# Kernel tuning notes

Measured on AMD Instinct MI355X. Metric: run time of the kernel, lower is better.

The kernel has to match this reference:

```python
import jax, jax.numpy as jnp
import numpy as np
import math

D = 64; H = 4; HD = 16; NL = 2; K = 3; FUT = 12; HID = 128
B = 8192; N = 16; L = 4; F = 7

def _linear(x, w, b):
    return x @ w.T + b

def _ln(x, g, b):
    m = x.mean(-1, keepdims=True)
    v = ((x - m) ** 2).mean(-1, keepdims=True)
    return (x - m) / jnp.sqrt(v + 1e-5) * g + b

def _mha(q, kv, in_w, in_b, out_w, out_b):
    # torch nn.MultiheadAttention: packed in_proj [Wq;Wk;Wv], averaged attn weights
    wq, wk, wv = in_w[:D], in_w[D:2*D], in_w[2*D:]
    bq, bk, bv = in_b[:D], in_b[D:2*D], in_b[2*D:]
    Bq, Lq, _ = q.shape; Lk = kv.shape[1]
    Q = (_linear(q, wq, bq)).reshape(Bq, Lq, H, HD)
    Kh = (_linear(kv, wk, bk)).reshape(Bq, Lk, H, HD)
    V = (_linear(kv, wv, bv)).reshape(Bq, Lk, H, HD)
    s = jnp.einsum('bqhd,bkhd->bhqk', Q, Kh) / math.sqrt(HD)
    a = jax.nn.softmax(s, axis=-1)
    o = jnp.einsum('bhqk,bkhd->bqhd', a, V).reshape(Bq, Lq, D)
    return _linear(o, out_w, out_b), a.mean(axis=1)

def _encode(tok, pe, embed_w, embed_b, layers):
    aiw, aib, aow, aob, f1w, f1b, f2w, f2b, l1g, l1b, l2g, l2b = layers
    x = _linear(tok, embed_w, embed_b) + pe[:, :tok.shape[1], :]
    for i in range(NL):
        a, _ = _mha(x, x, aiw[i], aib[i], aow[i], aob[i])
        x = _ln(x + a, l1g[i], l1b[i])
        f = _linear(jax.nn.relu(_linear(x, f1w[i], f1b[i])), f2w[i], f2b[i])
        x = _ln(x + f, l2g[i], l2b[i])
    return x[:, -1, :]

def _make_pe():
    pe = np.zeros((100, D), dtype=np.float32)
    pos = np.arange(100, dtype=np.float32)[:, None]
    div = np.exp(np.arange(0, D, 2, dtype=np.float32) * (-math.log(10000.0) / D))
    pe[:, 0::2] = np.sin(pos * div)
    pe[:, 1::2] = np.cos(pos * div)
    return jnp.asarray(pe[None])

def setup_inputs() -> dict:
    key = jax.random.key(0)
    ks = iter(jax.random.split(key, 40))
    p = lambda shape: jax.random.normal(next(ks), shape, dtype=jnp.float32) * 0.05
    inp = {
        'x': jax.random.normal(next(ks), (B, L, F), dtype=jnp.float32),
        'neighbors': jax.random.normal(next(ks), (B, N, L, F), dtype=jnp.float32),
        'pe': _make_pe(),
        'embed_w': p((D, F)), 'embed_b': p((D,)),
        'attn_in_w': p((NL, 3*D, D)), 'attn_in_b': p((NL, 3*D)),
        'attn_out_w': p((NL, D, D)), 'attn_out_b': p((NL, D)),
        'ff1_w': p((NL, 256, D)), 'ff1_b': p((NL, 256)),
        'ff2_w': p((NL, D, 256)), 'ff2_b': p((NL, D)),
        'ln1_g': jnp.ones((NL, D)), 'ln1_b': jnp.zeros((NL, D)),
        'ln2_g': jnp.ones((NL, D)), 'ln2_b': jnp.zeros((NL, D)),
        'soc_in_w': p((3*D, D)), 'soc_in_b': p((3*D,)),
        'soc_out_w': p((D, D)), 'soc_out_b': p((D,)),
        'goal1_w': p((64, HID)), 'goal1_b': p((64,)),
        'goal2_w': p((K*2, 64)), 'goal2_b': p((K*2,)),
        'traj1_w': p((128, HID + 2)), 'traj1_b': p((128,)),
        'traj2_w': p((FUT*2, 128)), 'traj2_b': p((FUT*2,)),
        'prob_w': p((K, HID)), 'prob_b': p((K,)),
    }
    return inp

def reference(x, neighbors, pe, embed_w, embed_b, attn_in_w, attn_in_b, attn_out_w, attn_out_b,
              ff1_w, ff1_b, ff2_w, ff2_b, ln1_g, ln1_b, ln2_g, ln2_b,
              soc_in_w, soc_in_b, soc_out_w, soc_out_b,
              goal1_w, goal1_b, goal2_w, goal2_b, traj1_w, traj1_b, traj2_w, traj2_b,
              prob_w, prob_b):
    b, n, l, f = neighbors.shape
    layers = (attn_in_w, attn_in_b, attn_out_w, attn_out_b, ff1_w, ff1_b, ff2_w, ff2_b,
              ln1_g, ln1_b, ln2_g, ln2_b)
    h = _encode(x, pe, embed_w, embed_b, layers)                       # (B, D) target last-token
    nh = _encode(neighbors.reshape(b*n, l, f), pe, embed_w, embed_b, layers).reshape(b, n, D)
    soc, attn_w = _mha(h[:, None, :], nh, soc_in_w, soc_in_b, soc_out_w, soc_out_b)
    h_final = jnp.concatenate([h, soc[:, 0, :]], axis=-1)              # (B, 128)
    goals = _linear(jax.nn.relu(_linear(h_final, goal1_w, goal1_b)), goal2_w, goal2_b).reshape(b, K, 2)
    cond = jnp.concatenate([jnp.broadcast_to(h_final[:, None, :], (b, K, HID)), goals], axis=-1)
    traj = _linear(jax.nn.relu(_linear(cond, traj1_w, traj1_b)), traj2_w, traj2_b).reshape(b, K, FUT, 2)
    probs = jax.nn.softmax(_linear(h_final, prob_w, prob_b), axis=-1)
    return traj, goals, probs, attn_w
```

## Files before the change

### kernel.cpp

```cpp
#include <hip/hip_runtime.h>

typedef __attribute__((ext_vector_type(8))) short short8;
typedef __attribute__((ext_vector_type(4))) float f32x4;

#define B_EGO 8192
#define NSEQ  139264

#define WS_CONST 0
#define WS_SIN   2432
#define WS_SOUT  14720
#define WS_G1    18816
#define WS_G2    27008
#define WS_T1    27392
#define WS_T1T   43776
#define WS_T2    44032
#define WS_PROB  47104
#define WS_H     47488
#define WS_NH    571776
#define PACK_F   8960384
#define PACK_HL  49152
#define PACK_PER_LAYER 98304

#define OUT_TRAJ  0
#define OUT_GOALS (B_EGO*72)
#define OUT_PROBS (OUT_GOALS + B_EGO*6)
#define OUT_ATTN  (OUT_PROBS + B_EGO*3)

#define MFMA(a,b,c) __builtin_amdgcn_mfma_f32_16x16x32_bf16(a,b,c,0,0,0)

__device__ __forceinline__ float dot4(float4 a, float4 b) {
  return a.x*b.x + a.y*b.y + a.z*b.z + a.w*b.w;
}
__device__ __forceinline__ unsigned short f2bf(float f) {
  unsigned int u = __float_as_uint(f);
  return (unsigned short)((u + 0x7FFFu + ((u >> 16) & 1u)) >> 16);
}
__device__ __forceinline__ float bfval(unsigned short h) {
  return __uint_as_float(((unsigned int)h) << 16);
}
__device__ __forceinline__ void pksplit(float a, float b,
                                        unsigned int& hi, unsigned int& lo) {
  unsigned int ua = __float_as_uint(a), ub = __float_as_uint(b);
  hi = (ua >> 16) | (ub & 0xFFFF0000u);
  float ra = a - __uint_as_float(ua & 0xFFFF0000u);
  float rb = b - __uint_as_float(ub & 0xFFFF0000u);
  unsigned short al = f2bf(ra), bl = f2bf(rb);
  lo = (unsigned int)al | ((unsigned int)bl << 16);
}
__device__ __forceinline__ short8 mkfrag(unsigned int a, unsigned int b,
                                         unsigned int c, unsigned int d) {
  union { short8 s; unsigned int w[4]; } u;
  u.w[0] = a; u.w[1] = b; u.w[2] = c; u.w[3] = d;
  return u.s;
}

__global__ void prep_consts(
    const float* __restrict__ embed_w, const float* __restrict__ embed_b,
    const float* __restrict__ pe,
    const float* __restrict__ attn_in_b, const float* __restrict__ attn_out_b,
    const float* __restrict__ ff1_b, const float* __restrict__ ff2_b,
    const float* __restrict__ ln1_g, const float* __restrict__ ln1_b,
    const float* __restrict__ ln2_g, const float* __restrict__ ln2_b,
    float* __restrict__ wsF)
{
  int idx = blockIdx.x * 256 + threadIdx.x;
  if (idx >= 2432) return;
  float v;
  if (idx < 448)      { int f = idx >> 6, c = idx & 63; v = embed_w[c*7 + f]; }
  else if (idx < 512) { v = embed_b[idx - 448]; }
  else if (idx < 768) { v = pe[idx - 512]; }
  else {
    int i = idx - 768, l = i / 832, j = i - l*832;
    if      (j < 192) v = attn_in_b [l*192 + j];
    else if (j < 256) v = attn_out_b[l*64  + j - 192];
    else if (j < 512) v = ff1_b     [l*256 + j - 256];
    else if (j < 576) v = ff2_b     [l*64  + j - 512];
    else if (j < 640) v = ln1_g     [l*64  + j - 576];
    else if (j < 704) v = ln1_b     [l*64  + j - 640];
    else if (j < 768) v = ln2_g     [l*64  + j - 704];
    else              v = ln2_b     [l*64  + j - 768];
  }
  wsF[idx] = v;
}

__global__ void prep_social(
    const float* __restrict__ soc_in_w, const float* __restrict__ soc_out_w,
    const float* __restrict__ goal1_w,  const float* __restrict__ goal2_w,
    const float* __restrict__ traj1_w,  const float* __restrict__ traj2_w,
    const float* __restrict__ prob_w,   float* __restrict__ wsF)
{
  int idx = blockIdx.x * 256 + threadIdx.x;
  if (idx >= 45056) return;
  float v; int t, i;
  if (idx < 12288) { t = idx; i = t & 3; t >>= 2; int o = t % 192, dc = t / 192;
    v = soc_in_w[o*64 + dc*4 + i]; }
  else if (idx < 16384) { t = idx - 12288; i = t & 3; t >>= 2; int o = t & 63, dc = t >> 6;
    v = soc_out_w[o*64 + dc*4 + i]; }
  else if (idx < 24576) { t = idx - 16384; i = t & 3; t >>= 2; int o = t & 63, dc = t >> 6;
    v = goal1_w[o*128 + dc*4 + i]; }
  else if (idx < 24960) { t = idx - 24576; i = t & 3; t >>= 2; int o = t % 6, dc = t / 6;
    v = goal2_w[o*64 + dc*4 + i]; }
  else if (idx < 41344) { t = idx - 24960; i = t & 3; t >>= 2; int o = t & 127, dc = t >> 7;
    v = traj1_w[o*130 + dc*4 + i]; }
  else if (idx < 41600) { t = idx - 41344; int o = t >> 1, j = t & 1;
    v = traj1_w[o*130 + 128 + j]; }
  else if (idx < 44672) { t = idx - 41600; i = t & 3; t >>= 2; int o = t % 24, dc = t / 24;
    v = traj2_w[o*128 + dc*4 + i]; }
  else { t = idx - 44672; i = t & 3; t >>= 2; int o = t % 3, dc = t / 3;
    v = prob_w[o*128 + dc*4 + i]; }
  wsF[WS_SIN + idx] = v;
}

__global__ void prep_mfma(
    const float* __restrict__ attn_in_w, const float* __restrict__ attn_out_w,
    const float* __restrict__ ff1_w,     const float* __restrict__ ff2_w,
    float* __restrict__ wsF)
{
  int idx = blockIdx.x * 256 + threadIdx.x;
  unsigned short* pw = (unsigned short*)(wsF + PACK_F);
  int l = idx / PACK_HL, r = idx - l*PACK_HL;
  int e = r & 7, lane = (r >> 3) & 63;
  int g = lane >> 4, l15 = lane & 15;
  float v;
  if (r < 12288) {
    int which = r >> 12;
    int ks = (r >> 9) & 1, t = (r >> 10) & 3;
    int c = (e & 3)*16 + ks*8 + 4*(e >> 2) + g;
    v = attn_in_w[l*12288 + (which*64 + t*16 + l15)*64 + c];
  } else if (r < 16384) {
    int r2 = r - 12288; int ks = (r2 >> 9) & 1, t = r2 >> 10;
    int c = ks*32 + g*4 + (e & 3) + 16*(e >> 2);
    v = attn_out_w[l*4096 + (t*16 + l15)*64 + c];
  } else if (r < 32768) {
    int r2 = r - 16384; int ks = (r2 >> 9) & 1, mt = r2 >> 10;
    int c = (e & 3)*16 + ks*8 + 4*(e >> 2) + g;
    v = ff1_w[l*16384 + (mt*16 + l15)*64 + c];
  } else {
    int r2 = r - 32768; int ks = (r2 >> 9) & 7, t = r2 >> 12;
    int c = ks*32 + g*4 + (e & 3) + 16*(e >> 2);
    v = ff2_w[l*16384 + (t*16 + l15)*256 + c];
  }
  unsigned short hw = f2bf(v);
  unsigned short lw = f2bf(v - bfval(hw));
  pw[l*PACK_PER_LAYER + r]           = hw;
  pw[l*PACK_PER_LAYER + PACK_HL + r] = lw;
}

__device__ __forceinline__ void lnorm(f32x4 xr[4], const float* cls,
                                      int gof, int bof, int l15) {
  float mean[4], rs[4];
  #pragma unroll
  for (int reg = 0; reg < 4; ++reg) {
    float s1 = xr[0][reg] + xr[1][reg] + xr[2][reg] + xr[3][reg];
    float s2 = xr[0][reg]*xr[0][reg] + xr[1][reg]*xr[1][reg]
             + xr[2][reg]*xr[2][reg] + xr[3][reg]*xr[3][reg];
    #pragma unroll
    for (int off = 1; off < 16; off <<= 1) {
      s1 += __shfl_xor(s1, off);
      s2 += __shfl_xor(s2, off);
    }
    float m = s1 * 0.015625f;
    float v = fmaxf(s2 * 0.015625f - m*m, 0.f);
    mean[reg] = m; rs[reg] = rsqrtf(v + 1e-5f);
  }
  #pragma unroll
  for (int t = 0; t < 4; ++t) {
    float gg = cls[gof + t*16 + l15], bb = cls[bof + t*16 + l15];
    #pragma unroll
    for (int reg = 0; reg < 4; ++reg)
      xr[t][reg] = (xr[t][reg] - mean[reg]) * rs[reg] * gg + bb;
  }
}

__device__ __forceinline__ void writeX(char* xbh, char* xbl,
                                       const f32x4 xr[4], int g, int l15) {
  #pragma unroll
  for (int reg = 0; reg < 4; ++reg) {
    int r = g*4 + reg;
    uint2 vh, vl;
    pksplit(xr[0][reg], xr[1][reg], vh.x, vl.x);
    pksplit(xr[2][reg], xr[3][reg], vh.y, vl.y);
    int off = (r*128 + l15*8) ^ ((r & 7) << 4);
    *(uint2*)(xbh + off) = vh;
    *(uint2*)(xbl + off) = vl;
  }
}

__device__ __forceinline__ void readX(const char* xbh, const char* xbl,
                                      short8 xah[2], short8 xal[2],
                                      int g, int l15) {
  #pragma unroll
  for (int ks = 0; ks < 2; ++ks) {
    int o1 = (l15*128 + ks*64 + g*8)      ^ ((l15 & 7) << 4);
    int o2 = (l15*128 + ks*64 + g*8 + 32) ^ ((l15 & 7) << 4);
    union { short8 s; uint2 d[2]; } uh, ul;
    uh.d[0] = *(const uint2*)(xbh + o1); uh.d[1] = *(const uint2*)(xbh + o2);
    ul.d[0] = *(const uint2*)(xbl + o1); ul.d[1] = *(const uint2*)(xbl + o2);
    xah[ks] = uh.s; xal[ks] = ul.s;
  }
}

__device__ __forceinline__ void splitA(const f32x4 a, const f32x4 b,
                                       short8& fh, short8& fl) {
  unsigned int w0, w1, w2, w3, z0, z1, z2, z3;
  pksplit(a[0], a[1], w0, z0);
  pksplit(a[2], a[3], w1, z1);
  pksplit(b[0], b[1], w2, z2);
  pksplit(b[2], b[3], w3, z3);
  fh = mkfrag(w0, w1, w2, w3);
  fl = mkfrag(z0, z1, z2, z3);
}

__global__ __launch_bounds__(256) void encode_kernel(
    const float* __restrict__ xin, const float* __restrict__ nbr,
    const float* __restrict__ wsF, float* __restrict__ hout)
{
  __shared__ __align__(16) float cls[2432];
  __shared__ float tok_ls[4][112];
  __shared__ __align__(16) unsigned short xs[4][2048];

  const int tid = threadIdx.x;
  const int w = tid >> 6, lane = tid & 63;
  const int g = lane >> 4, l15 = lane & 15;
  const f32x4 zero = {0.f, 0.f, 0.f, 0.f};

  for (int i = tid; i < 2432; i += 256) cls[i] = wsF[i];

  const int seq0w = blockIdx.x * 16 + w * 4;
  {
    const float* tokp = (blockIdx.x < 512) ? (xin + seq0w*28)
                                           : (nbr + (seq0w - B_EGO)*28);
    tok_ls[w][lane] = tokp[lane];
    if (lane < 48) tok_ls[w][64 + lane] = tokp[64 + lane];
  }
  __syncthreads();

  char* xbh = (char*)(xs[w]);
  char* xbl = xbh + 2048;
  const unsigned short* pw = (const unsigned short*)(wsF + PACK_F);

  f32x4 xr[4];
  {
    float tk[4][7];
    #pragma unroll
    for (int reg = 0; reg < 4; ++reg)
      #pragma unroll
      for (int f = 0; f < 7; ++f)
        tk[reg][f] = tok_ls[w][g*28 + reg*7 + f];
    #pragma unroll
    for (int t = 0; t < 4; ++t) {
      const int c = t*16 + l15;
      float we[7];
      #pragma unroll
      for (int f = 0; f < 7; ++f) we[f] = cls[f*64 + c];
      const float ebv = cls[448 + c];
      #pragma unroll
      for (int reg = 0; reg < 4; ++reg) {
        float acc = ebv + cls[512 + reg*64 + c];
        #pragma unroll
        for (int f = 0; f < 7; ++f) acc = fmaf(tk[reg][f], we[f], acc);
        xr[t][reg] = acc;
      }
    }
  }
  writeX(xbh, xbl, xr, g, l15);

  #pragma unroll 1
  for (int ly = 0; ly < 2; ++ly) {
    const unsigned short* PLh = pw + ly*PACK_PER_LAYER;
    const unsigned short* PLl = PLh + PACK_HL;
    const int lb = 768 + ly*832;
    short8 xah[2], xal[2];
    readX(xbh, xbl, xah, xal, g, l15);

    f32x4 q4[4], k4[4], v4[4];
    #pragma unroll
    for (int t = 0; t < 4; ++t) {
      q4[t] = zero; k4[t] = zero; v4[t] = zero;
      #pragma unroll
      for (int ks = 0; ks < 2; ++ks) {
        const int wo = ((t*2+ks)*64 + lane)*8;
        short8 aqh = *(const short8*)(PLh + wo);
        short8 aql = *(const short8*)(PLl + wo);
        short8 akh = *(const short8*)(PLh + 4096 + wo);
        short8 akl = *(const short8*)(PLl + 4096 + wo);
        short8 bvh = *(const short8*)(PLh + 8192 + wo);
        short8 bvl = *(const short8*)(PLl + 8192 + wo);
        q4[t] = MFMA(aql, xah[ks], MFMA(aqh, xal[ks], MFMA(aqh, xah[ks], q4[t])));
        k4[t] = MFMA(akl, xah[ks], MFMA(akh, xal[ks], MFMA(akh, xah[ks], k4[t])));
        v4[t] = MFMA(xal[ks], bvh, MFMA(xah[ks], bvl, MFMA(xah[ks], bvh, v4[t])));
      }
      f32x4 bq = *(const f32x4*)(&cls[lb +      t*16 + g*4]);
      f32x4 bk = *(const f32x4*)(&cls[lb + 64 + t*16 + g*4]);
      q4[t] += bq; k4[t] += bk;
      float bvv = cls[lb + 128 + t*16 + l15];
      #pragma unroll
      for (int j = 0; j < 4; ++j) v4[t][j] += bvv;
    }

    f32x4 oacc[4];
    const float vmask = (g == (l15 >> 2)) ? 1.f : 0.f;
    #pragma unroll
    for (int h = 0; h < 4; ++h) {
      short8 aKh, aKl, bQh, bQl;
      splitA(k4[h], zero, aKh, aKl);
      splitA(q4[h], zero, bQh, bQl);
      f32x4 sa = MFMA(aKl, bQh, MFMA(aKh, bQl, MFMA(aKh, bQh, zero)));
      float s0 = sa[0]*0.25f, s1 = sa[1]*0.25f, s2 = sa[2]*0.25f, s3 = sa[3]*0.25f;
      float mx = fmaxf(fmaxf(s0, s1), fmaxf(s2, s3));
      float e0 = __expf(s0-mx), e1 = __expf(s1-mx), e2 = __expf(s2-mx), e3 = __expf(s3-mx);
      float inv = vmask / (e0 + e1 + e2 + e3);
      f32x4 pv = {e0*inv, e1*inv, e2*inv, e3*inv};
      short8 aVh, aVl, bPh, bPl;
      splitA(v4[h], zero, aVh, aVl);
      splitA(pv,    zero, bPh, bPl);
      oacc[h] = MFMA(aVl, bPh, MFMA(aVh, bPl, MFMA(aVh, bPh, zero)));
    }

    short8 aOh[2], aOl[2];
    #pragma unroll
    for (int ks = 0; ks < 2; ++ks)
      splitA(oacc[2*ks], oacc[2*ks+1], aOh[ks], aOl[ks]);
    #pragma unroll
    for (int t = 0; t < 4; ++t) {
      f32x4 fa = zero;
      #pragma unroll
      for (int ks = 0; ks < 2; ++ks) {
        const int wo = 12288 + ((t*2+ks)*64 + lane)*8;
        short8 bOh = *(const short8*)(PLh + wo);
        short8 bOl = *(const short8*)(PLl + wo);
        fa = MFMA(aOl[ks], bOh, MFMA(aOh[ks], bOl, MFMA(aOh[ks], bOh, fa)));
      }
      float bo = cls[lb + 192 + t*16 + l15];
      #pragma unroll
      for (int j = 0; j < 4; ++j) xr[t][j] += fa[j] + bo;
    }
    lnorm(xr, cls, lb + 576, lb + 640, l15);

    writeX(xbh, xbl, xr, g, l15);
    readX(xbh, xbl, xah, xal, g, l15);

    f32x4 h16[16];
    #pragma unroll
    for (int mt = 0; mt < 16; ++mt) {
      h16[mt] = zero;
      #pragma unroll
      for (int ks = 0; ks < 2; ++ks) {
        const int wo = 16384 + ((mt*2+ks)*64 + lane)*8;
        short8 a1h = *(const short8*)(PLh + wo);
        short8 a1l = *(const short8*)(PLl + wo);
        h16[mt] = MFMA(a1l, xah[ks], MFMA(a1h, xal[ks], MFMA(a1h, xah[ks], h16[mt])));
      }
      f32x4 b1 = *(const f32x4*)(&cls[lb + 256 + mt*16 + g*4]);
      #pragma unroll
      for (int j = 0; j < 4; ++j) h16[mt][j] = fmaxf(h16[mt][j] + b1[j], 0.f);
    }

    f32x4 f2[4] = {zero, zero, zero, zero};
    #pragma unroll
    for (int ks = 0; ks < 8; ++ks) {
      short8 aHh, aHl;
      splitA(h16[2*ks], h16[2*ks+1], aHh, aHl);
      #pragma unroll
      for (int t = 0; t < 4; ++t) {
        const int wo = 32768 + ((t*8+ks)*64 + lane)*8;
        short8 b2h = *(const short8*)(PLh + wo);
        short8 b2l = *(const short8*)(PLl + wo);
        f2[t] = MFMA(aHl, b2h, MFMA(aHh, b2l, MFMA(aHh, b2h, f2[t])));
      }
    }
    #pragma unroll
    for (int t = 0; t < 4; ++t) {
      float b2v = cls[lb + 512 + t*16 + l15];
      #pragma unroll
      for (int j = 0; j < 4; ++j) xr[t][j] += f2[t][j] + b2v;
    }
    lnorm(xr, cls, lb + 704, lb + 768, l15);

    writeX(xbh, xbl, xr, g, l15);
  }

  #pragma unroll
  for (int t = 0; t < 4; ++t)
    hout[(seq0w + g)*64 + t*16 + l15] = xr[t][3];
}

__global__ __launch_bounds__(256) void social_head_kernel(
    const float* __restrict__ ws,
    const float* __restrict__ soc_in_b, const float* __restrict__ soc_out_b,
    const float* __restrict__ goal1_b,  const float* __restrict__ goal2_b,
    const float* __restrict__ traj1_b,  const float* __restrict__ traj2_b,
    const float* __restrict__ prob_b,
    float* __restrict__ out)
{
  const float*  h    = ws + WS_H;
  const float*  nhp  = ws + WS_NH;
  const float4* sInP  = reinterpret_cast<const float4*>(ws + WS_SIN);
  const float4* sOutP = reinterpret_cast<const float4*>(ws + WS_SOUT);
  const float4* g1P   = reinterpret_cast<const float4*>(ws + WS_G1);
  const float4* g2P   = reinterpret_cast<const float4*>(ws + WS_G2);
  const float4* t1P   = reinterpret_cast<const float4*>(ws + WS_T1);
  const float*  t1T   = ws + WS_T1T;
  const float4* t2P   = reinterpret_cast<const float4*>(ws + WS_T2);
  const float4* pP    = reinterpret_cast<const float4*>(ws + WS_PROB);

  __shared__ __align__(16) float nls[4][16][64];
  __shared__ __align__(16) float kls[4][16][64];
  __shared__ __align__(16) float hfls[4][128];
  __shared__ __align__(16) float qls[4][64];
  __shared__ float als[4][64];
  __shared__ __align__(16) float ovls[4][64];
  __shared__ __align__(16) float g1ls[4][64];
  __shared__ __align__(16) float t1ls[4][128];
  __shared__ float gls[4][8];
  __shared__ float pls[4][4];

  const int w = threadIdx.x >> 6, lane = threadIdx.x & 63;
  const int b = blockIdx.x * 4 + w;

  hfls[w][lane] = h[b*64 + lane];
  #pragma unroll
  for (int t = 0; t < 16; ++t)
    nls[w][t][lane] = nhp[b*1024 + t*64 + lane];
  __syncthreads();

  float Q = soc_in_b[lane];
  #pragma unroll 4
  for (int dc = 0; dc < 16; ++dc)
    Q += dot4(*reinterpret_cast<const float4*>(&hfls[w][dc*4]), sInP[dc*192 + lane]);

  float Kv[16], Vv[16];
  {
    float bk = soc_in_b[64 + lane], bv = soc_in_b[128 + lane];
    #pragma unroll
    for (int k = 0; k < 16; ++k) { Kv[k] = bk; Vv[k] = bv; }
  }
  #pragma unroll 4
  for (int dc = 0; dc < 16; ++dc) {
    float4 wk = sInP[dc*192 + 64  + lane];
    float4 wv = sInP[dc*192 + 128 + lane];
    #pragma unroll
    for (int k = 0; k < 16; ++k) {
      float4 nv = *reinterpret_cast<const float4*>(&nls[w][k][dc*4]);
      Kv[k] += dot4(nv, wk);
      Vv[k] += dot4(nv, wv);
    }
  }
  qls[w][lane] = Q;
  #pragma unroll
  for (int k = 0; k < 16; ++k) kls[w][k][lane] = Kv[k];
  __syncthreads();

  {
    const int shh = lane >> 4, kk = lane & 15;
    float sc = 0.f;
    #pragma unroll
    for (int hd = 0; hd < 16; ++hd)
      sc += qls[w][shh*16 + hd] * kls[w][kk][shh*16 + hd];
    sc *= 0.25f;
    float m = sc;
    #pragma unroll
    for (int off = 1; off < 16; off <<= 1) m = fmaxf(m, __shfl_xor(m, off));
    float e = __expf(sc - m);
    float sm = e;
    #pragma unroll
    for (int off = 1; off < 16; off <<= 1) sm += __shfl_xor(sm, off);
    float a = e / sm;
    als[w][lane] = a;
    float am = a + __shfl_xor(a, 16);
    am += __shfl_xor(am, 32);
    if (lane < 16) out[OUT_ATTN + b*16 + lane] = 0.25f * am;
  }
  __syncthreads();

  {
    float ov = 0.f;
    #pragma unroll
    for (int k = 0; k < 16; ++k)
      ov += als[w][(lane & ~15) + k] * Vv[k];
    ovls[w][lane] = ov;
  }
  __syncthreads();
  {
    float soc = soc_out_b[lane];
    #pragma unroll 4
    for (int dc = 0; dc < 16; ++dc)
      soc += dot4(*reinterpret_cast<const float4*>(&ovls[w][dc*4]), sOutP[dc*64 + lane]);
    hfls[w][64 + lane] = soc;
  }
  __syncthreads();

  {
    float g1 = goal1_b[lane];
    #pragma unroll 4
    for (int dc = 0; dc < 32; ++dc)
      g1 += dot4(*reinterpret_cast<const float4*>(&hfls[w][dc*4]), g1P[dc*64 + lane]);
    g1ls[w][lane] = fmaxf(g1, 0.f);
  }
  __syncthreads();

  if (lane < 6) {
    float gv = goal2_b[lane];
    #pragma unroll 4
    for (int dc = 0; dc < 16; ++dc)
      gv += dot4(*reinterpret_cast<const float4*>(&g1ls[w][dc*4]), g2P[dc*6 + lane]);
    gls[w][lane] = gv;
    out[OUT_GOALS + b*6 + lane] = gv;
  } else if (lane >= 8 && lane < 11) {
    const int o = lane - 8;
    float pv = prob_b[o];
    #pragma unroll 4
    for (int dc = 0; dc < 32; ++dc)
      pv += dot4(*reinterpret_cast<const float4*>(&hfls[w][dc*4]), pP[dc*3 + o]);
    pls[w][o] = pv;
  }
  __syncthreads();
  if (lane < 3) {
    float p0 = pls[w][0], p1 = pls[w][1], p2 = pls[w][2];
    float mx = fmaxf(p0, fmaxf(p1, p2));
    float e0 = __expf(p0 - mx), e1 = __expf(p1 - mx), e2 = __expf(p2 - mx);
    float mine = (lane == 0) ? e0 : ((lane == 1) ? e1 : e2);
    out[OUT_PROBS + b*3 + lane] = mine / (e0 + e1 + e2);
  }

  for (int k3 = 0; k3 < 3; ++k3) {
    const float gx = gls[w][k3*2], gy = gls[w][k3*2 + 1];
    float t0 = traj1_b[lane], t1v = traj1_b[64 + lane];
    #pragma unroll 4
    for (int dc = 0; dc < 32; ++dc) {
      float4 xv = *reinterpret_cast<const float4*>(&hfls[w][dc*4]);
      t0  += dot4(xv, t1P[dc*128 + lane]);
      t1v += dot4(xv, t1P[dc*128 + 64 + lane]);
    }
    t0  += gx * t1T[lane*2]      + gy * t1T[lane*2 + 1];
    t1v += gx * t1T[(64+lane)*2] + gy * t1T[(64+lane)*2 + 1];
    t1ls[w][lane]      = fmaxf(t0, 0.f);
    t1ls[w][64 + lane] = fmaxf(t1v, 0.f);
    __syncthreads();
    if (lane < 24) {
      float tv = traj2_b[lane];
      #pragma unroll 4
      for (int dc = 0; dc < 32; ++dc)
        tv += dot4(*reinterpret_cast<const float4*>(&t1ls[w][dc*4]), t2P[dc*24 + lane]);
      out[OUT_TRAJ + b*72 + k3*24 + lane] = tv;
    }
    __syncthreads();
  }
}

extern "C" void kernel_launch(void* const* d_in, const int* in_sizes, int n_in,
                              void* d_out, int out_size, void* d_ws, size_t ws_size,
                              hipStream_t stream) {
  const float* xin        = (const float*)d_in[0];
  const float* neighbors  = (const float*)d_in[1];
  const float* pe         = (const float*)d_in[2];
  const float* embed_w    = (const float*)d_in[3];
  const float* embed_b    = (const float*)d_in[4];
  const float* attn_in_w  = (const float*)d_in[5];
  const float* attn_in_b  = (const float*)d_in[6];
  const float* attn_out_w = (const float*)d_in[7];
  const float* attn_out_b = (const float*)d_in[8];
  const float* ff1_w      = (const float*)d_in[9];
  const float* ff1_b      = (const float*)d_in[10];
  const float* ff2_w      = (const float*)d_in[11];
  const float* ff2_b      = (const float*)d_in[12];
  const float* ln1_g      = (const float*)d_in[13];
  const float* ln1_b      = (const float*)d_in[14];
  const float* ln2_g      = (const float*)d_in[15];
  const float* ln2_b      = (const float*)d_in[16];
  const float* soc_in_w   = (const float*)d_in[17];
  const float* soc_in_b   = (const float*)d_in[18];
  const float* soc_out_w  = (const float*)d_in[19];
  const float* soc_out_b  = (const float*)d_in[20];
  const float* goal1_w    = (const float*)d_in[21];
  const float* goal1_b    = (const float*)d_in[22];
  const float* goal2_w    = (const float*)d_in[23];
  const float* goal2_b    = (const float*)d_in[24];
  const float* traj1_w    = (const float*)d_in[25];
  const float* traj1_b    = (const float*)d_in[26];
  const float* traj2_w    = (const float*)d_in[27];
  const float* traj2_b    = (const float*)d_in[28];
  const float* prob_w     = (const float*)d_in[29];
  const float* prob_b     = (const float*)d_in[30];

  float* ws  = (float*)d_ws;
  float* out = (float*)d_out;

  prep_consts<<<10, 256, 0, stream>>>(embed_w, embed_b, pe, attn_in_b,
      attn_out_b, ff1_b, ff2_b, ln1_g, ln1_b, ln2_g, ln2_b, ws);
  prep_social<<<176, 256, 0, stream>>>(soc_in_w, soc_out_w, goal1_w, goal2_w,
      traj1_w, traj2_w, prob_w, ws);
  prep_mfma<<<384, 256, 0, stream>>>(attn_in_w, attn_out_w, ff1_w, ff2_w, ws);

  encode_kernel<<<NSEQ/16, 256, 0, stream>>>(xin, neighbors, ws, ws + WS_H);

  social_head_kernel<<<B_EGO/4, 256, 0, stream>>>(
      ws, soc_in_b, soc_out_b, goal1_b, goal2_b, traj1_b, traj2_b, prob_b, out);
}
```

Baseline: 841.6 us.

## Process two sequence groups per wave to reuse weight fragments across MFMAs

Each wave now encodes 8 sequences (two sets of 4) instead of 4, so every weight fragment loaded from global memory feeds MFMAs for both sets. The grid is halved to match. The FFN is also restructured to compute hidden tiles in pairs inside a non-unrolled loop and consume them right away, rather than holding all 16 hidden tiles in registers. This cuts weight-load traffic per sequence and limits FFN register pressure, but doubles the other per-wave state and LDS use, which may lower occupancy.

```diff
diff --git a/kernel.cpp b/kernel.cpp
--- a/kernel.cpp
+++ b/kernel.cpp
@@ -216,8 +216,8 @@
     const float* __restrict__ wsF, float* __restrict__ hout)
 {
   __shared__ __align__(16) float cls[2432];
-  __shared__ float tok_ls[4][112];
-  __shared__ __align__(16) unsigned short xs[4][2048];
+  __shared__ float tok_ls[4][224];
+  __shared__ __align__(16) unsigned short xs[4][2][2048];
 
   const int tid = threadIdx.x;
   const int w = tid >> 6, lane = tid & 63;
@@ -226,27 +226,29 @@
 
   for (int i = tid; i < 2432; i += 256) cls[i] = wsF[i];
 
-  const int seq0w = blockIdx.x * 16 + w * 4;
+  const int seq0w = blockIdx.x * 32 + w * 8;
   {
-    const float* tokp = (blockIdx.x < 512) ? (xin + seq0w*28)
+    const float* tokp = (blockIdx.x < 256) ? (xin + seq0w*28)
                                            : (nbr + (seq0w - B_EGO)*28);
-    tok_ls[w][lane] = tokp[lane];
-    if (lane < 48) tok_ls[w][64 + lane] = tokp[64 + lane];
-  }
-  __syncthreads();
-
-  char* xbh = (char*)(xs[w]);
-  char* xbl = xbh + 2048;
+    tok_ls[w][lane]       = tokp[lane];
+    tok_ls[w][64 + lane]  = tokp[64 + lane];
+    tok_ls[w][128 + lane] = tokp[128 + lane];
+    if (lane < 32) tok_ls[w][192 + lane] = tokp[192 + lane];
+  }
+  __syncthreads();
+
+  char* xb[2] = { (char*)xs[w][0], (char*)xs[w][1] };
   const unsigned short* pw = (const unsigned short*)(wsF + PACK_F);
 
-  f32x4 xr[4];
-  {
+  f32x4 xr[2][4];
+  #pragma unroll
+  for (int s = 0; s < 2; ++s) {
     float tk[4][7];
     #pragma unroll
     for (int reg = 0; reg < 4; ++reg)
       #pragma unroll
       for (int f = 0; f < 7; ++f)
-        tk[reg][f] = tok_ls[w][g*28 + reg*7 + f];
+        tk[reg][f] = tok_ls[w][s*112 + g*28 + reg*7 + f];
     #pragma unroll
     for (int t = 0; t < 4; ++t) {
       const int c = t*16 + l15;
@@ -259,24 +261,27 @@
         float acc = ebv + cls[512 + reg*64 + c];
         #pragma unroll
         for (int f = 0; f < 7; ++f) acc = fmaf(tk[reg][f], we[f], acc);
-        xr[t][reg] = acc;
-      }
-    }
-  }
-  writeX(xbh, xbl, xr, g, l15);
+        xr[s][t][reg] = acc;
+      }
+    }
+    writeX(xb[s], xb[s] + 2048, xr[s], g, l15);
+  }
 
   #pragma unroll 1
   for (int ly = 0; ly < 2; ++ly) {
     const unsigned short* PLh = pw + ly*PACK_PER_LAYER;
     const unsigned short* PLl = PLh + PACK_HL;
     const int lb = 768 + ly*832;
-    short8 xah[2], xal[2];
-    readX(xbh, xbl, xah, xal, g, l15);
-
-    f32x4 q4[4], k4[4], v4[4];
+    short8 xah[2][2], xal[2][2];
+    #pragma unroll
+    for (int s = 0; s < 2; ++s)
+      readX(xb[s], xb[s] + 2048, xah[s], xal[s], g, l15);
+
+    f32x4 q4[2][4], k4[2][4], v4[2][4];
     #pragma unroll
     for (int t = 0; t < 4; ++t) {
-      q4[t] = zero; k4[t] = zero; v4[t] = zero;
+      #pragma unroll
+      for (int s = 0; s < 2; ++s) { q4[s][t] = zero; k4[s][t] = zero; v4[s][t] = zero; }
       #pragma unroll
       for (int ks = 0; ks < 2; ++ks) {
         const int wo = ((t*2+ks)*64 + lane)*8;
@@ -286,103 +291,135 @@
         short8 akl = *(const short8*)(PLl + 4096 + wo);
         short8 bvh = *(const short8*)(PLh + 8192 + wo);
         short8 bvl = *(const short8*)(PLl + 8192 + wo);
-        q4[t] = MFMA(aql, xah[ks], MFMA(aqh, xal[ks], MFMA(aqh, xah[ks], q4[t])));
-        k4[t] = MFMA(akl, xah[ks], MFMA(akh, xal[ks], MFMA(akh, xah[ks], k4[t])));
-        v4[t] = MFMA(xal[ks], bvh, MFMA(xah[ks], bvl, MFMA(xah[ks], bvh, v4[t])));
+        #pragma unroll
+        for (int s = 0; s < 2; ++s) {
+          q4[s][t] = MFMA(aql, xah[s][ks], MFMA(aqh, xal[s][ks], MFMA(aqh, xah[s][ks], q4[s][t])));
+          k4[s][t] = MFMA(akl, xah[s][ks], MFMA(akh, xal[s][ks], MFMA(akh, xah[s][ks], k4[s][t])));
+          v4[s][t] = MFMA(xal[s][ks], bvh, MFMA(xah[s][ks], bvl, MFMA(xah[s][ks], bvh, v4[s][t])));
+        }
       }
       f32x4 bq = *(const f32x4*)(&cls[lb +      t*16 + g*4]);
       f32x4 bk = *(const f32x4*)(&cls[lb + 64 + t*16 + g*4]);
-      q4[t] += bq; k4[t] += bk;
       float bvv = cls[lb + 128 + t*16 + l15];
       #pragma unroll
-      for (int j = 0; j < 4; ++j) v4[t][j] += bvv;
-    }
-
-    f32x4 oacc[4];
+      for (int s = 0; s < 2; ++s) {
+        q4[s][t] += bq; k4[s][t] += bk;
+        #pragma unroll
+        for (int j = 0; j < 4; ++j) v4[s][t][j] += bvv;
+      }
+    }
+
+    f32x4 oacc[2][4];
     const float vmask = (g == (l15 >> 2)) ? 1.f : 0.f;
     #pragma unroll
-    for (int h = 0; h < 4; ++h) {
-      short8 aKh, aKl, bQh, bQl;
-      splitA(k4[h], zero, aKh, aKl);
-      splitA(q4[h], zero, bQh, bQl);
-      f32x4 sa = MFMA(aKl, bQh, MFMA(aKh, bQl, MFMA(aKh, bQh, zero)));
-      float s0 = sa[0]*0.25f, s1 = sa[1]*0.25f, s2 = sa[2]*0.25f, s3 = sa[3]*0.25f;
-      float mx = fmaxf(fmaxf(s0, s1), fmaxf(s2, s3));
-      float e0 = __expf(s0-mx), e1 = __expf(s1-mx), e2 = __expf(s2-mx), e3 = __expf(s3-mx);
-      float inv = vmask / (e0 + e1 + e2 + e3);
-      f32x4 pv = {e0*inv, e1*inv, e2*inv, e3*inv};
-      short8 aVh, aVl, bPh, bPl;
-      splitA(v4[h], zero, aVh, aVl);
-      splitA(pv,    zero, bPh, bPl);
-      oacc[h] = MFMA(aVl, bPh, MFMA(aVh, bPl, MFMA(aVh, bPh, zero)));
-    }
-
-    short8 aOh[2], aOl[2];
-    #pragma unroll
-    for (int ks = 0; ks < 2; ++ks)
-      splitA(oacc[2*ks], oacc[2*ks+1], aOh[ks], aOl[ks]);
+    for (int s = 0; s < 2; ++s) {
+      #pragma unroll
+      for (int h = 0; h < 4; ++h) {
+        short8 aKh, aKl, bQh, bQl;
+        splitA(k4[s][h], zero, aKh, aKl);
+        splitA(q4[s][h], zero, bQh, bQl);
+        f32x4 sa = MFMA(aKl, bQh, MFMA(aKh, bQl, MFMA(aKh, bQh, zero)));
+        float s0 = sa[0]*0.25f, s1 = sa[1]*0.25f, s2 = sa[2]*0.25f, s3 = sa[3]*0.25f;
+        float mx = fmaxf(fmaxf(s0, s1), fmaxf(s2, s3));
+        float e0 = __expf(s0-mx), e1 = __expf(s1-mx), e2 = __expf(s2-mx), e3 = __expf(s3-mx);
+        float inv = vmask / (e0 + e1 + e2 + e3);
+        f32x4 pv = {e0*inv, e1*inv, e2*inv, e3*inv};
+        short8 aVh, aVl, bPh, bPl;
+        splitA(v4[s][h], zero, aVh, aVl);
+        splitA(pv,       zero, bPh, bPl);
+        oacc[s][h] = MFMA(aVl, bPh, MFMA(aVh, bPl, MFMA(aVh, bPh, zero)));
+      }
+    }
+
+    short8 aOh[2][2], aOl[2][2];
+    #pragma unroll
+    for (int s = 0; s < 2; ++s)
+      #pragma unroll
+      for (int ks = 0; ks < 2; ++ks)
+        splitA(oacc[s][2*ks], oacc[s][2*ks+1], aOh[s][ks], aOl[s][ks]);
     #pragma unroll
     for (int t = 0; t < 4; ++t) {
-      f32x4 fa = zero;
+      f32x4 fa[2] = {zero, zero};
       #pragma unroll
       for (int ks = 0; ks < 2; ++ks) {
         const int wo = 12288 + ((t*2+ks)*64 + lane)*8;
         short8 bOh = *(const short8*)(PLh + wo);
         short8 bOl = *(const short8*)(PLl + wo);
-        fa = MFMA(aOl[ks], bOh, MFMA(aOh[ks], bOl, MFMA(aOh[ks], bOh, fa)));
+        #pragma unroll
+        for (int s = 0; s < 2; ++s)
+          fa[s] = MFMA(aOl[s][ks], bOh, MFMA(aOh[s][ks], bOl, MFMA(aOh[s][ks], bOh, fa[s])));
       }
       float bo = cls[lb + 192 + t*16 + l15];
       #pragma unroll
-      for (int j = 0; j < 4; ++j) xr[t][j] += fa[j] + bo;
-    }
-    lnorm(xr, cls, lb + 576, lb + 640, l15);
-
-    writeX(xbh, xbl, xr, g, l15);
-    readX(xbh, xbl, xah, xal, g, l15);
-
-    f32x4 h16[16];
-    #pragma unroll
-    for (int mt = 0; mt < 16; ++mt) {
-      h16[mt] = zero;
+      for (int s = 0; s < 2; ++s)
+        #pragma unroll
+        for (int j = 0; j < 4; ++j) xr[s][t][j] += fa[s][j] + bo;
+    }
+    #pragma unroll
+    for (int s = 0; s < 2; ++s) {
+      lnorm(xr[s], cls, lb + 576, lb + 640, l15);
+      writeX(xb[s], xb[s] + 2048, xr[s], g, l15);
+      readX(xb[s], xb[s] + 2048, xah[s], xal[s], g, l15);
+    }
+
+    f32x4 f2[2][4] = {{zero, zero, zero, zero}, {zero, zero, zero, zero}};
+    #pragma unroll 1
+    for (int ks8 = 0; ks8 < 8; ++ks8) {
+      f32x4 ha[2] = {zero, zero}, hb[2] = {zero, zero};
       #pragma unroll
       for (int ks = 0; ks < 2; ++ks) {
-        const int wo = 16384 + ((mt*2+ks)*64 + lane)*8;
-        short8 a1h = *(const short8*)(PLh + wo);
-        short8 a1l = *(const short8*)(PLl + wo);
-        h16[mt] = MFMA(a1l, xah[ks], MFMA(a1h, xal[ks], MFMA(a1h, xah[ks], h16[mt])));
-      }
-      f32x4 b1 = *(const f32x4*)(&cls[lb + 256 + mt*16 + g*4]);
-      #pragma unroll
-      for (int j = 0; j < 4; ++j) h16[mt][j] = fmaxf(h16[mt][j] + b1[j], 0.f);
-    }
-
-    f32x4 f2[4] = {zero, zero, zero, zero};
-    #pragma unroll
-    for (int ks = 0; ks < 8; ++ks) {
-      short8 aHh, aHl;
-      splitA(h16[2*ks], h16[2*ks+1], aHh, aHl);
+        const int woa = 16384 + (((2*ks8  )*2+ks)*64 + lane)*8;
+        const int wob = 16384 + (((2*ks8+1)*2+ks)*64 + lane)*8;
+        short8 a1h = *(const short8*)(PLh + woa);
+        short8 a1l = *(const short8*)(PLl + woa);
+        short8 b1h = *(const short8*)(PLh + wob);
+        short8 b1l = *(const short8*)(PLl + wob);
+        #pragma unroll
+        for (int s = 0; s < 2; ++s) {
+          ha[s] = MFMA(a1l, xah[s][ks], MFMA(a1h, xal[s][ks], MFMA(a1h, xah[s][ks], ha[s])));
+          hb[s] = MFMA(b1l, xah[s][ks], MFMA(b1h, xal[s][ks], MFMA(b1h, xah[s][ks], hb[s])));
+        }
+      }
+      f32x4 ba = *(const f32x4*)(&cls[lb + 256 + (2*ks8  )*16 + g*4]);
+      f32x4 bb = *(const f32x4*)(&cls[lb + 256 + (2*ks8+1)*16 + g*4]);
+      short8 aHh[2], aHl[2];
+      #pragma unroll
+      for (int s = 0; s < 2; ++s) {
+        #pragma unroll
+        for (int j = 0; j < 4; ++j) {
+          ha[s][j] = fmaxf(ha[s][j] + ba[j], 0.f);
+          hb[s][j] = fmaxf(hb[s][j] + bb[j], 0.f);
+        }
+        splitA(ha[s], hb[s], aHh[s], aHl[s]);
+      }
       #pragma unroll
       for (int t = 0; t < 4; ++t) {
-        const int wo = 32768 + ((t*8+ks)*64 + lane)*8;
+        const int wo = 32768 + ((t*8+ks8)*64 + lane)*8;
         short8 b2h = *(const short8*)(PLh + wo);
         short8 b2l = *(const short8*)(PLl + wo);
-        f2[t] = MFMA(aHl, b2h, MFMA(aHh, b2l, MFMA(aHh, b2h, f2[t])));
-      }
-    }
-    #pragma unroll
-    for (int t = 0; t < 4; ++t) {
-      float b2v = cls[lb + 512 + t*16 + l15];
-      #pragma unroll
-      for (int j = 0; j < 4; ++j) xr[t][j] += f2[t][j] + b2v;
-    }
-    lnorm(xr, cls, lb + 704, lb + 768, l15);
-
-    writeX(xbh, xbl, xr, g, l15);
-  }
-
-  #pragma unroll
-  for (int t = 0; t < 4; ++t)
-    hout[(seq0w + g)*64 + t*16 + l15] = xr[t][3];
+        #pragma unroll
+        for (int s = 0; s < 2; ++s)
+          f2[s][t] = MFMA(aHl[s], b2h, MFMA(aHh[s], b2l, MFMA(aHh[s], b2h, f2[s][t])));
+      }
+    }
+    #pragma unroll
+    for (int s = 0; s < 2; ++s) {
+      #pragma unroll
+      for (int t = 0; t < 4; ++t) {
+        float b2v = cls[lb + 512 + t*16 + l15];
+        #pragma unroll
+        for (int j = 0; j < 4; ++j) xr[s][t][j] += f2[s][t][j] + b2v;
+      }
+      lnorm(xr[s], cls, lb + 704, lb + 768, l15);
+      writeX(xb[s], xb[s] + 2048, xr[s], g, l15);
+    }
+  }
+
+  #pragma unroll
+  for (int s = 0; s < 2; ++s)
+    #pragma unroll
+    for (int t = 0; t < 4; ++t)
+      hout[(seq0w + s*4 + g)*64 + t*16 + l15] = xr[s][t][3];
 }
 
 __global__ __launch_bounds__(256) void social_head_kernel(
@@ -592,7 +629,7 @@
       traj1_w, traj2_w, prob_w, ws);
   prep_mfma<<<384, 256, 0, stream>>>(attn_in_w, attn_out_w, ff1_w, ff2_w, ws);
 
-  encode_kernel<<<NSEQ/16, 256, 0, stream>>>(xin, neighbors, ws, ws + WS_H);
+  encode_kernel<<<NSEQ/32, 256, 0, stream>>>(xin, neighbors, ws, ws + WS_H);
 
   social_head_kernel<<<B_EGO/4, 256, 0, stream>>>(
       ws, soc_in_b, soc_out_b, goal1_b, goal2_b, traj1_b, traj2_b, prob_b, out);
```

New measurement: 898.8 us. +6.8%, slower.
